# Kernel tuning notes

Hardware: AMD Instinct MI355X
Metric: run time of the kernel (lower is better)

## Reference

```python
import jax, jax.numpy as jnp
import numpy as np


def _l2_normalize(v, axis, eps=1e-12):
    # matches F.normalize / cosine_similarity denominator clamping
    n = jnp.linalg.norm(v, axis=axis, keepdims=True)
    return v / jnp.maximum(n, eps)


def setup_inputs() -> dict:
    key = jax.random.key(0)
    k1, k2, k3 = jax.random.split(key, 3)
    B, D, C = 65536, 1024, 4
    x = jax.random.normal(k1, (B, D), dtype=jnp.float32)
    label = jax.random.randint(k2, (B,), 0, C, dtype=jnp.int64)
    text_concept = jax.random.normal(k3, (C, D), dtype=jnp.float32)
    concept_flag = 2
    return {"x": x, "label": label, "text_concept": text_concept, "concept_flag": concept_flag}


def reference(x, label, text_concept, concept_flag):
    B = x.shape[0]
    x = x.reshape(B, x.shape[1])
    # F.normalize(x, dim=1); cosine_similarity then re-normalizes (idempotent for x)
    xn = _l2_normalize(x, axis=1)            # [B, D]
    tn = _l2_normalize(text_concept, axis=1)  # [4, D]
    # per-sample: sim = cos(x_i, text_concept)  -> batched matmul [B, 4]
    sim = jnp.einsum('bd,cd->bc', xn, tn)
    # exp(sim[flag]) / sum(exp(sim)) == softmax over concepts, pick flag column
    probs = jax.nn.softmax(sim, axis=1)      # [B, 4]
    loss = jnp.mean(probs[:, concept_flag])
    return loss
```

## Files before the change

kernel.cpp:

```cpp
#include <hip/hip_runtime.h>
#include <math.h>

#define B_ROWS 65536
#define DIM    1024
#define NCON   4
#define NBLK   1024

__global__ void __launch_bounds__(256, 4) sim_kernel(const float* __restrict__ x,
                                                     const float* __restrict__ tc,
                                                     const int*   __restrict__ flag_ptr,
                                                     float*       __restrict__ partials) {
    const int wid  = threadIdx.x >> 6;
    const int lane = threadIdx.x & 63;

    float4 t[NCON][4];
#pragma unroll
    for (int c = 0; c < NCON; ++c) {
        float ss = 0.f;
#pragma unroll
        for (int it = 0; it < 4; ++it) {
            t[c][it] = *reinterpret_cast<const float4*>(tc + c * DIM + it * 256 + lane * 4);
            ss += t[c][it].x * t[c][it].x + t[c][it].y * t[c][it].y
                + t[c][it].z * t[c][it].z + t[c][it].w * t[c][it].w;
        }
#pragma unroll
        for (int m = 32; m >= 1; m >>= 1) ss += __shfl_xor(ss, m);
        const float inv = 1.f / fmaxf(sqrtf(ss), 1e-12f);
#pragma unroll
        for (int it = 0; it < 4; ++it) {
            t[c][it].x *= inv; t[c][it].y *= inv; t[c][it].z *= inv; t[c][it].w *= inv;
        }
    }

    const int flag = *flag_ptr;

    constexpr int ROWS_PER_WAVE = B_ROWS / (NBLK * 4);
    const int    gw      = blockIdx.x * 4 + wid;
    const size_t rstride = (size_t)(NBLK * 4) * DIM;
    const float* xr      = x + (size_t)gw * DIM + lane * 4;

    float4 cur[4], nxt[4];
#pragma unroll
    for (int it = 0; it < 4; ++it)
        cur[it] = *reinterpret_cast<const float4*>(xr + it * 256);

    float wsum = 0.f;
#pragma unroll 2
    for (int i = 0; i < ROWS_PER_WAVE; ++i) {
        if (i + 1 < ROWS_PER_WAVE) {
            const float* xn = xr + (size_t)(i + 1) * rstride;
#pragma unroll
            for (int it = 0; it < 4; ++it)
                nxt[it] = *reinterpret_cast<const float4*>(xn + it * 256);
        }

        float acc0 = 0.f, acc1 = 0.f, acc2 = 0.f, acc3 = 0.f, xx = 0.f;
#pragma unroll
        for (int it = 0; it < 4; ++it) {
            const float4 v = cur[it];
            xx   += v.x * v.x        + v.y * v.y        + v.z * v.z        + v.w * v.w;
            acc0 += v.x * t[0][it].x + v.y * t[0][it].y + v.z * t[0][it].z + v.w * t[0][it].w;
            acc1 += v.x * t[1][it].x + v.y * t[1][it].y + v.z * t[1][it].z + v.w * t[1][it].w;
            acc2 += v.x * t[2][it].x + v.y * t[2][it].y + v.z * t[2][it].z + v.w * t[2][it].w;
            acc3 += v.x * t[3][it].x + v.y * t[3][it].y + v.z * t[3][it].z + v.w * t[3][it].w;
        }
#pragma unroll
        for (int m = 32; m >= 1; m >>= 1) {
            xx   += __shfl_xor(xx,   m);
            acc0 += __shfl_xor(acc0, m);
            acc1 += __shfl_xor(acc1, m);
            acc2 += __shfl_xor(acc2, m);
            acc3 += __shfl_xor(acc3, m);
        }
        if (lane == 0) {
            const float inv = 1.f / fmaxf(sqrtf(xx), 1e-12f);
            const float s0 = acc0 * inv, s1 = acc1 * inv, s2 = acc2 * inv, s3 = acc3 * inv;
            const float mx = fmaxf(fmaxf(s0, s1), fmaxf(s2, s3));
            const float e0 = __expf(s0 - mx), e1 = __expf(s1 - mx),
                        e2 = __expf(s2 - mx), e3 = __expf(s3 - mx);
            const float esum = e0 + e1 + e2 + e3;
            const float sel  = (flag == 0) ? e0 : (flag == 1) ? e1 : (flag == 2) ? e2 : e3;
            wsum += sel / esum;
        }

        if (i + 1 < ROWS_PER_WAVE) {
#pragma unroll
            for (int it = 0; it < 4; ++it) cur[it] = nxt[it];
        }
    }

    __shared__ float ls[4];
    if (lane == 0) ls[wid] = wsum;
    __syncthreads();
    if (threadIdx.x == 0) partials[blockIdx.x] = ls[0] + ls[1] + ls[2] + ls[3];
}

__global__ void reduce_kernel(const float* __restrict__ partials, float* __restrict__ out) {
    __shared__ double ls[256];
    double s = 0.0;
    for (int i = threadIdx.x; i < NBLK; i += 256) s += (double)partials[i];
    ls[threadIdx.x] = s;
    __syncthreads();
    for (int st = 128; st >= 1; st >>= 1) {
        if (threadIdx.x < st) ls[threadIdx.x] += ls[threadIdx.x + st];
        __syncthreads();
    }
    if (threadIdx.x == 0) out[0] = (float)(ls[0] / (double)B_ROWS);
}

extern "C" void kernel_launch(void* const* d_in, const int* in_sizes, int n_in,
                              void* d_out, int out_size, void* d_ws, size_t ws_size,
                              hipStream_t stream) {
    const float* x    = (const float*)d_in[0];
    const float* tc   = (const float*)d_in[2];
    const int*   flag = (const int*)d_in[3];
    float* out = (float*)d_out;

    float* partials = (float*)d_ws;

    sim_kernel<<<NBLK, 256, 0, stream>>>(x, tc, flag, partials);
    reduce_kernel<<<1, 256, 0, stream>>>(partials, out);
}
```

Baseline: 49.61 us.

## Fuse final reduction via last-block atomic counter and use nontemporal loads

```diff
diff --git a/kernel.cpp b/kernel.cpp
--- a/kernel.cpp
+++ b/kernel.cpp
@@ -6,30 +6,32 @@
 #define NCON   4
 #define NBLK   1024
 
+typedef float vf4 __attribute__((ext_vector_type(4)));
+
 __global__ void __launch_bounds__(256, 4) sim_kernel(const float* __restrict__ x,
                                                      const float* __restrict__ tc,
                                                      const int*   __restrict__ flag_ptr,
-                                                     float*       __restrict__ partials) {
+                                                     float*       __restrict__ partials,
+                                                     unsigned*    __restrict__ counter,
+                                                     float*       __restrict__ out) {
     const int wid  = threadIdx.x >> 6;
     const int lane = threadIdx.x & 63;
 
-    float4 t[NCON][4];
+    vf4 t[NCON][4];
 #pragma unroll
     for (int c = 0; c < NCON; ++c) {
         float ss = 0.f;
 #pragma unroll
         for (int it = 0; it < 4; ++it) {
-            t[c][it] = *reinterpret_cast<const float4*>(tc + c * DIM + it * 256 + lane * 4);
-            ss += t[c][it].x * t[c][it].x + t[c][it].y * t[c][it].y
-                + t[c][it].z * t[c][it].z + t[c][it].w * t[c][it].w;
+            t[c][it] = *reinterpret_cast<const vf4*>(tc + c * DIM + it * 256 + lane * 4);
+            ss += t[c][it][0] * t[c][it][0] + t[c][it][1] * t[c][it][1]
+                + t[c][it][2] * t[c][it][2] + t[c][it][3] * t[c][it][3];
         }
 #pragma unroll
         for (int m = 32; m >= 1; m >>= 1) ss += __shfl_xor(ss, m);
         const float inv = 1.f / fmaxf(sqrtf(ss), 1e-12f);
 #pragma unroll
-        for (int it = 0; it < 4; ++it) {
-            t[c][it].x *= inv; t[c][it].y *= inv; t[c][it].z *= inv; t[c][it].w *= inv;
-        }
+        for (int it = 0; it < 4; ++it) t[c][it] *= inv;
     }
 
     const int flag = *flag_ptr;
@@ -39,10 +41,10 @@
     const size_t rstride = (size_t)(NBLK * 4) * DIM;
     const float* xr      = x + (size_t)gw * DIM + lane * 4;
 
-    float4 cur[4], nxt[4];
+    vf4 cur[4], nxt[4];
 #pragma unroll
     for (int it = 0; it < 4; ++it)
-        cur[it] = *reinterpret_cast<const float4*>(xr + it * 256);
+        cur[it] = __builtin_nontemporal_load(reinterpret_cast<const vf4*>(xr + it * 256));
 
     float wsum = 0.f;
 #pragma unroll 2
@@ -51,18 +53,21 @@
             const float* xn = xr + (size_t)(i + 1) * rstride;
 #pragma unroll
             for (int it = 0; it < 4; ++it)
-                nxt[it] = *reinterpret_cast<const float4*>(xn + it * 256);
+                nxt[it] = __builtin_nontemporal_load(reinterpret_cast<const vf4*>(xn + it * 256));
         }
 
         float acc0 = 0.f, acc1 = 0.f, acc2 = 0.f, acc3 = 0.f, xx = 0.f;
 #pragma unroll
         for (int it = 0; it < 4; ++it) {
-            const float4 v = cur[it];
-            xx   += v.x * v.x        + v.y * v.y        + v.z * v.z        + v.w * v.w;
-            acc0 += v.x * t[0][it].x + v.y * t[0][it].y + v.z * t[0][it].z + v.w * t[0][it].w;
-            acc1 += v.x * t[1][it].x + v.y * t[1][it].y + v.z * t[1][it].z + v.w * t[1][it].w;
-            acc2 += v.x * t[2][it].x + v.y * t[2][it].y + v.z * t[2][it].z + v.w * t[2][it].w;
-            acc3 += v.x * t[3][it].x + v.y * t[3][it].y + v.z * t[3][it].z + v.w * t[3][it].w;
+            const vf4 v = cur[it];
+#pragma unroll
+            for (int e = 0; e < 4; ++e) {
+                xx   += v[e] * v[e];
+                acc0 += v[e] * t[0][it][e];
+                acc1 += v[e] * t[1][it][e];
+                acc2 += v[e] * t[2][it][e];
+                acc3 += v[e] * t[3][it][e];
+            }
         }
 #pragma unroll
         for (int m = 32; m >= 1; m >>= 1) {
@@ -90,22 +95,29 @@
     }
 
     __shared__ float ls[4];
+    __shared__ bool  amLast;
     if (lane == 0) ls[wid] = wsum;
     __syncthreads();
-    if (threadIdx.x == 0) partials[blockIdx.x] = ls[0] + ls[1] + ls[2] + ls[3];
-}
+    if (threadIdx.x == 0) {
+        const float p = ls[0] + ls[1] + ls[2] + ls[3];
+        __hip_atomic_store(&partials[blockIdx.x], p, __ATOMIC_RELEASE, __HIP_MEMORY_SCOPE_AGENT);
+        const unsigned old = __hip_atomic_fetch_add(counter, 1u, __ATOMIC_ACQ_REL, __HIP_MEMORY_SCOPE_AGENT);
+        amLast = (old == NBLK - 1);
+    }
+    __syncthreads();
+    if (!amLast) return;
 
-__global__ void reduce_kernel(const float* __restrict__ partials, float* __restrict__ out) {
-    __shared__ double ls[256];
     double s = 0.0;
-    for (int i = threadIdx.x; i < NBLK; i += 256) s += (double)partials[i];
-    ls[threadIdx.x] = s;
+    for (int i = threadIdx.x; i < NBLK; i += 256)
+        s += (double)__hip_atomic_load(&partials[i], __ATOMIC_RELAXED, __HIP_MEMORY_SCOPE_AGENT);
+    __shared__ double ds[256];
+    ds[threadIdx.x] = s;
     __syncthreads();
     for (int st = 128; st >= 1; st >>= 1) {
-        if (threadIdx.x < st) ls[threadIdx.x] += ls[threadIdx.x + st];
+        if (threadIdx.x < st) ds[threadIdx.x] += ds[threadIdx.x + st];
         __syncthreads();
     }
-    if (threadIdx.x == 0) out[0] = (float)(ls[0] / (double)B_ROWS);
+    if (threadIdx.x == 0) out[0] = (float)(ds[0] / (double)B_ROWS);
 }
 
 extern "C" void kernel_launch(void* const* d_in, const int* in_sizes, int n_in,
@@ -116,8 +128,9 @@
     const int*   flag = (const int*)d_in[3];
     float* out = (float*)d_out;
 
-    float* partials = (float*)d_ws;
+    float*    partials = (float*)d_ws;
+    unsigned* counter  = (unsigned*)((char*)d_ws + 4096);
 
-    sim_kernel<<<NBLK, 256, 0, stream>>>(x, tc, flag, partials);
-    reduce_kernel<<<1, 256, 0, stream>>>(partials, out);
+    hipMemsetAsync(counter, 0, sizeof(unsigned), stream);
+    sim_kernel<<<NBLK, 256, 0, stream>>>(x, tc, flag, partials, counter, out);
 }
```

Result: slower. 127.6 us (+157.2%).
